# Kernel optimization log

Hardware: AMD Instinct MI355X
Metric: run time of the kernel (lower is better)

## Reference

```python
import jax, jax.numpy as jnp
import numpy as np

TAU = 0.07
EPS = 1e-6  # torch CosineSimilarity eps


def setup_inputs() -> dict:
    key = jax.random.key(0)
    k1, k2, k3 = jax.random.split(key, 3)
    n, d, n_classes = 8192, 256, 1024
    imitation_embeds = jax.random.normal(k1, (n, d), dtype=jnp.float32)
    recording_embeds = jax.random.normal(k2, (n, d), dtype=jnp.float32)
    labels = jax.random.randint(k3, (n,), 0, n_classes, dtype=jnp.int64)
    return {
        "imitation_embeds": imitation_embeds,
        "recording_embeds": recording_embeds,
        "labels": labels,
    }


def reference(imitation_embeds, recording_embeds, labels):
    n = imitation_embeds.shape[0]
    # cosine similarity with per-vector norm clamp (torch semantics)
    im_n = imitation_embeds / jnp.maximum(
        jnp.linalg.norm(imitation_embeds, axis=1, keepdims=True), EPS)
    rec_n = recording_embeds / jnp.maximum(
        jnp.linalg.norm(recording_embeds, axis=1, keepdims=True), EPS)
    i2r = jnp.einsum("nd,md->nm", im_n, rec_n) / TAU  # [n, n]

    same = labels[:, None] == labels[None, :]          # [n, n] bool
    eye = jnp.eye(n, dtype=bool)
    # original: mask = ~(same ^ diag_embed(diag(same))); diag(same) is all True
    # -> keep the diagonal (positive) and all different-label negatives
    mask = ~(same ^ eye)

    # per-row masked log-softmax evaluated at the diagonal entry:
    # log_softmax(row[mask])[pos_of_diag] = i2r[i,i] - logsumexp(row over mask)
    lse = jax.nn.logsumexp(jnp.where(mask, i2r, -jnp.inf), axis=1)  # [n]
    loss = -jnp.mean(jnp.diagonal(i2r) - lse)
    return loss
```

## Files before the change

kernel.cpp:

```cpp
#include <hip/hip_runtime.h>

#define N 8192
#define D 256
#define INV_TAU 14.285714285714286f
#define LOG2E 1.4426950408889634f
#define EPSN 1e-6f

#define RT 256
#define CT 32
#define CSPLIT 16
#define CPB (N / CSPLIT)
#define NTILES (CPB / CT)
#define MAXC 96

typedef unsigned int u32x4 __attribute__((ext_vector_type(4)));
typedef __bf16 bf16x8 __attribute__((ext_vector_type(8)));
typedef float f32x4 __attribute__((ext_vector_type(4)));

__device__ inline unsigned short f2bf(float x) {
    unsigned int u = __builtin_bit_cast(unsigned int, x);
    u += 0x7fffu + ((u >> 16) & 1u);
    return (unsigned short)(u >> 16);
}

__device__ inline float bf2f(unsigned short u) {
    return __builtin_bit_cast(float, (unsigned int)u << 16);
}

__global__ void ntx_prep(const float* __restrict__ im, const float* __restrict__ rec,
                         unsigned short* __restrict__ A, unsigned short* __restrict__ Bm,
                         float* __restrict__ diag, float* __restrict__ rowsum,
                         int* __restrict__ cnt, float* __restrict__ out) {
    const int wave = threadIdx.x >> 6;
    const int lane = threadIdx.x & 63;
    const int row  = blockIdx.x * 4 + wave;

    const float4 a = ((const float4*)(im  + (size_t)row * D))[lane];
    const float4 b = ((const float4*)(rec + (size_t)row * D))[lane];

    float ssa = a.x*a.x + a.y*a.y + a.z*a.z + a.w*a.w;
    float ssb = b.x*b.x + b.y*b.y + b.z*b.z + b.w*b.w;
    float dt  = a.x*b.x + a.y*b.y + a.z*b.z + a.w*b.w;
    #pragma unroll
    for (int o = 32; o; o >>= 1) {
        ssa += __shfl_xor(ssa, o);
        ssb += __shfl_xor(ssb, o);
        dt  += __shfl_xor(dt , o);
    }
    const float ra = 1.0f / fmaxf(sqrtf(ssa), EPSN);
    const float rb = 1.0f / fmaxf(sqrtf(ssb), EPSN);
    const float sa = ra * (INV_TAU * LOG2E);

    ushort4 pa, pb;
    pa.x = f2bf(a.x*sa); pa.y = f2bf(a.y*sa); pa.z = f2bf(a.z*sa); pa.w = f2bf(a.w*sa);
    pb.x = f2bf(b.x*rb); pb.y = f2bf(b.y*rb); pb.z = f2bf(b.z*rb); pb.w = f2bf(b.w*rb);
    *(ushort4*)(A  + (size_t)row * D + lane * 4) = pa;
    *(ushort4*)(Bm + (size_t)row * D + lane * 4) = pb;

    if (lane == 0) {
        diag[row]   = dt * ra * rb * INV_TAU;
        rowsum[row] = 0.0f;
    }
    if (blockIdx.x < 4) cnt[blockIdx.x * 256 + threadIdx.x] = 0;
    if (blockIdx.x == 0 && threadIdx.x == 0) out[0] = 0.0f;
}

__global__ void ntx_bucket(const int* __restrict__ labels, int* __restrict__ cnt,
                           int* __restrict__ bucket) {
    const int i = blockIdx.x * 256 + threadIdx.x;
    const int c = labels[i];
    const int pos = atomicAdd(&cnt[c], 1);
    if (pos < MAXC) bucket[c * MAXC + pos] = i;
}

__global__ void ntx_pairs(const unsigned short* __restrict__ A,
                          const unsigned short* __restrict__ Bm,
                          const int* __restrict__ labels,
                          const int* __restrict__ cnt, const int* __restrict__ bucket,
                          float* __restrict__ rowsum) {
    const int wave = threadIdx.x >> 6;
    const int lane = threadIdx.x & 63;
    const int i = blockIdx.x * 4 + wave;
    const int c = labels[i];
    const int m = min(cnt[c], MAXC);
    if (m < 2) return;

    const ushort4 av = *(const ushort4*)(A + (size_t)i * D + lane * 4);
    const float a0 = bf2f(av.x), a1 = bf2f(av.y), a2 = bf2f(av.z), a3 = bf2f(av.w);

    int jr_n = bucket[c * MAXC];
    ushort4 bv_n = *(const ushort4*)(Bm + (size_t)jr_n * D + lane * 4);

    float corr = 0.f;
    for (int j = 0; j < m; ++j) {
        const int jr = jr_n;
        const ushort4 bv = bv_n;
        if (j + 1 < m) {
            jr_n = bucket[c * MAXC + j + 1];
            bv_n = *(const ushort4*)(Bm + (size_t)jr_n * D + lane * 4);
        }
        if (jr == i) continue;
        float d = a0*bf2f(bv.x) + a1*bf2f(bv.y) + a2*bf2f(bv.z) + a3*bf2f(bv.w);
        #pragma unroll
        for (int o = 32; o; o >>= 1) d += __shfl_xor(d, o);
        corr += __builtin_amdgcn_exp2f(d);
    }
    if (lane == 0) atomicAdd(&rowsum[i], -corr);
}

__device__ __forceinline__ void stage_tile4(const unsigned short* __restrict__ Bm,
                                            int colt, int wave, int lane,
                                            unsigned char* lb) {
    const int g = lane >> 4, n16 = lane & 15;
    #pragma unroll
    for (int p = 0; p < 4; ++p) {
        const int csk = wave * 4 + p;
        const int cs = csk >> 3, k = csk & 7;
        const unsigned short* gs =
            Bm + (size_t)(colt + cs * 16 + n16) * D + k * 32 + g * 8;
        __builtin_amdgcn_global_load_lds(
            (const __attribute__((address_space(1))) unsigned int*)gs,
            (__attribute__((address_space(3))) unsigned int*)(lb + csk * 1024),
            16, 0, 0);
    }
}

template<bool STAGE>
__device__ __forceinline__ void tile_step(const unsigned short* __restrict__ Bm,
                                          int colstage, int wave, int lane,
                                          const unsigned char* cur, unsigned char* stg,
                                          const bf16x8 (&afrag)[4][8], float (&acc)[4][4]) {
    const int g = lane >> 4, n16 = lane & 15;
    #pragma unroll
    for (int cs = 0; cs < 2; ++cs) {
        if constexpr (STAGE) {
            #pragma unroll
            for (int p = cs * 2; p < cs * 2 + 2; ++p) {
                const int csk = wave * 4 + p;
                const int scs = csk >> 3, sk = csk & 7;
                const unsigned short* gs =
                    Bm + (size_t)(colstage + scs * 16 + n16) * D + sk * 32 + g * 8;
                __builtin_amdgcn_global_load_lds(
                    (const __attribute__((address_space(1))) unsigned int*)gs,
                    (__attribute__((address_space(3))) unsigned int*)(stg + csk * 1024),
                    16, 0, 0);
            }
        }
        bf16x8 bfrag[8];
        #pragma unroll
        for (int k = 0; k < 8; ++k)
            bfrag[k] = __builtin_bit_cast(
                bf16x8, *(const u32x4*)(cur + (cs * 8 + k) * 1024 + lane * 16));

        f32x4 c[4];
        __builtin_amdgcn_s_setprio(1);
        #pragma unroll
        for (int rs = 0; rs < 4; ++rs) {
            c[rs] = (f32x4){0.f, 0.f, 0.f, 0.f};
            #pragma unroll
            for (int k = 0; k < 8; ++k)
                c[rs] = __builtin_amdgcn_mfma_f32_16x16x32_bf16(
                            afrag[rs][k], bfrag[k], c[rs], 0, 0, 0);
        }
        __builtin_amdgcn_s_setprio(0);
        #pragma unroll
        for (int rs = 0; rs < 4; ++rs)
            #pragma unroll
            for (int q = 0; q < 4; ++q)
                acc[rs][q] += __builtin_amdgcn_exp2f(c[rs][q]);
    }
}

__global__ __launch_bounds__(256, 2)
void ntx_lse(const unsigned short* __restrict__ A, const unsigned short* __restrict__ Bm,
             float* __restrict__ rowsum) {
    __shared__ __align__(128) unsigned char Bs[3][CT * 512];

    const int wave = threadIdx.x >> 6;
    const int lane = threadIdx.x & 63;
    const int g    = lane >> 4;
    const int n16  = lane & 15;

    const int rowblk = blockIdx.x & (N / RT - 1);
    const int colblk = blockIdx.x >> 5;
    const int row0 = rowblk * RT + wave * 64;
    const int col0 = colblk * CPB;

    bf16x8 afrag[4][8];
    #pragma unroll
    for (int rs = 0; rs < 4; ++rs) {
        const int r = row0 + rs * 16 + n16;
        #pragma unroll
        for (int k = 0; k < 8; ++k)
            afrag[rs][k] = __builtin_bit_cast(
                bf16x8, *(const u32x4*)(A + (size_t)r * D + k * 32 + g * 8));
    }

    float acc[4][4];
    #pragma unroll
    for (int rs = 0; rs < 4; ++rs)
        #pragma unroll
        for (int q = 0; q < 4; ++q) acc[rs][q] = 0.f;

    unsigned char* b0 = &Bs[0][0];
    unsigned char* b1 = &Bs[1][0];
    unsigned char* b2 = &Bs[2][0];

    stage_tile4(Bm, col0,      wave, lane, b0);
    stage_tile4(Bm, col0 + CT, wave, lane, b1);

    for (int t = 0; t < NTILES - 1; ++t) {
        asm volatile("s_waitcnt vmcnt(4)" ::: "memory");
        __builtin_amdgcn_s_barrier();
        __builtin_amdgcn_sched_barrier(0);

        if (t + 2 < NTILES)
            tile_step<true >(Bm, col0 + (t + 2) * CT, wave, lane, b0, b2, afrag, acc);
        else
            tile_step<false>(Bm, 0, wave, lane, b0, b2, afrag, acc);

        unsigned char* tmp = b0; b0 = b1; b1 = b2; b2 = tmp;
    }
    asm volatile("s_waitcnt vmcnt(0)" ::: "memory");
    __builtin_amdgcn_s_barrier();
    __builtin_amdgcn_sched_barrier(0);
    tile_step<false>(Bm, 0, wave, lane, b0, b2, afrag, acc);

    #pragma unroll
    for (int rs = 0; rs < 4; ++rs)
        #pragma unroll
        for (int q = 0; q < 4; ++q) {
            float v = acc[rs][q];
            v += __shfl_xor(v, 1);
            v += __shfl_xor(v, 2);
            v += __shfl_xor(v, 4);
            v += __shfl_xor(v, 8);
            if (n16 == 0)
                atomicAdd(&rowsum[row0 + rs * 16 + g * 4 + q], v);
        }
}

__global__ void ntx_finish(const float* __restrict__ diag,
                           const float* __restrict__ rowsum,
                           float* __restrict__ out) {
    __shared__ float red[4];
    const int i = blockIdx.x * 256 + threadIdx.x;
    float s = logf(rowsum[i]) - diag[i];
    #pragma unroll
    for (int o = 32; o; o >>= 1) s += __shfl_xor(s, o);
    if ((threadIdx.x & 63) == 0) red[threadIdx.x >> 6] = s;
    __syncthreads();
    if (threadIdx.x == 0)
        atomicAdd(out, (red[0] + red[1] + red[2] + red[3]) * (1.0f / (float)N));
}

extern "C" void kernel_launch(void* const* d_in, const int* in_sizes, int n_in,
                              void* d_out, int out_size, void* d_ws, size_t ws_size,
                              hipStream_t stream) {
    const float* im     = (const float*)d_in[0];
    const float* rec    = (const float*)d_in[1];
    const int*   labels = (const int*)d_in[2];
    float* out = (float*)d_out;

    unsigned short* A  = (unsigned short*)d_ws;
    unsigned short* Bm = A + (size_t)N * D;
    float* diag   = (float*)(Bm + (size_t)N * D);
    float* rowsum = diag + N;
    int*   cnt    = (int*)(rowsum + N);
    int*   bucket = cnt + 1024;

    ntx_prep<<<N / 4, 256, 0, stream>>>(im, rec, A, Bm, diag, rowsum, cnt, out);
    ntx_bucket<<<N / 256, 256, 0, stream>>>(labels, cnt, bucket);
    ntx_pairs<<<N / 4, 256, 0, stream>>>(A, Bm, labels, cnt, bucket, rowsum);
    ntx_lse<<<(N / RT) * CSPLIT, 256, 0, stream>>>(A, Bm, rowsum);
    ntx_finish<<<N / 256, 256, 0, stream>>>(diag, rowsum, out);
}
```

Before: 121.0 us.

## Halve rows per wave and interleave MFMAs across column subtiles

```diff
diff --git a/kernel.cpp b/kernel.cpp
--- a/kernel.cpp
+++ b/kernel.cpp
@@ -6,9 +6,9 @@
 #define LOG2E 1.4426950408889634f
 #define EPSN 1e-6f
 
-#define RT 256
+#define RT 128
 #define CT 32
-#define CSPLIT 16
+#define CSPLIT 8
 #define CPB (N / CSPLIT)
 #define NTILES (CPB / CT)
 #define MAXC 96
@@ -129,46 +129,55 @@
 __device__ __forceinline__ void tile_step(const unsigned short* __restrict__ Bm,
                                           int colstage, int wave, int lane,
                                           const unsigned char* cur, unsigned char* stg,
-                                          const bf16x8 (&afrag)[4][8], float (&acc)[4][4]) {
+                                          const bf16x8 (&afrag)[2][8], float (&acc)[2][4]) {
     const int g = lane >> 4, n16 = lane & 15;
-    #pragma unroll
-    for (int cs = 0; cs < 2; ++cs) {
-        if constexpr (STAGE) {
+    if constexpr (STAGE) {
+        #pragma unroll
+        for (int p = 0; p < 4; ++p) {
+            const int csk = wave * 4 + p;
+            const int scs = csk >> 3, sk = csk & 7;
+            const unsigned short* gs =
+                Bm + (size_t)(colstage + scs * 16 + n16) * D + sk * 32 + g * 8;
+            __builtin_amdgcn_global_load_lds(
+                (const __attribute__((address_space(1))) unsigned int*)gs,
+                (__attribute__((address_space(3))) unsigned int*)(stg + csk * 1024),
+                16, 0, 0);
+        }
+    }
+
+    bf16x8 bfrag[2][8];
+    #pragma unroll
+    for (int cs = 0; cs < 2; ++cs)
+        #pragma unroll
+        for (int k = 0; k < 8; ++k)
+            bfrag[cs][k] = __builtin_bit_cast(
+                bf16x8, *(const u32x4*)(cur + (cs * 8 + k) * 1024 + lane * 16));
+
+    f32x4 c[2][2];
+    #pragma unroll
+    for (int cs = 0; cs < 2; ++cs)
+        #pragma unroll
+        for (int rs = 0; rs < 2; ++rs)
+            c[cs][rs] = (f32x4){0.f, 0.f, 0.f, 0.f};
+
+    __builtin_amdgcn_s_setprio(1);
+    #pragma unroll
+    for (int k = 0; k < 8; ++k)
+        #pragma unroll
+        for (int cs = 0; cs < 2; ++cs)
             #pragma unroll
-            for (int p = cs * 2; p < cs * 2 + 2; ++p) {
-                const int csk = wave * 4 + p;
-                const int scs = csk >> 3, sk = csk & 7;
-                const unsigned short* gs =
-                    Bm + (size_t)(colstage + scs * 16 + n16) * D + sk * 32 + g * 8;
-                __builtin_amdgcn_global_load_lds(
-                    (const __attribute__((address_space(1))) unsigned int*)gs,
-                    (__attribute__((address_space(3))) unsigned int*)(stg + csk * 1024),
-                    16, 0, 0);
-            }
-        }
-        bf16x8 bfrag[8];
-        #pragma unroll
-        for (int k = 0; k < 8; ++k)
-            bfrag[k] = __builtin_bit_cast(
-                bf16x8, *(const u32x4*)(cur + (cs * 8 + k) * 1024 + lane * 16));
-
-        f32x4 c[4];
-        __builtin_amdgcn_s_setprio(1);
-        #pragma unroll
-        for (int rs = 0; rs < 4; ++rs) {
-            c[rs] = (f32x4){0.f, 0.f, 0.f, 0.f};
-            #pragma unroll
-            for (int k = 0; k < 8; ++k)
-                c[rs] = __builtin_amdgcn_mfma_f32_16x16x32_bf16(
-                            afrag[rs][k], bfrag[k], c[rs], 0, 0, 0);
-        }
-        __builtin_amdgcn_s_setprio(0);
-        #pragma unroll
-        for (int rs = 0; rs < 4; ++rs)
+            for (int rs = 0; rs < 2; ++rs)
+                c[cs][rs] = __builtin_amdgcn_mfma_f32_16x16x32_bf16(
+                                afrag[rs][k], bfrag[cs][k], c[cs][rs], 0, 0, 0);
+    __builtin_amdgcn_s_setprio(0);
+
+    #pragma unroll
+    for (int cs = 0; cs < 2; ++cs)
+        #pragma unroll
+        for (int rs = 0; rs < 2; ++rs)
             #pragma unroll
             for (int q = 0; q < 4; ++q)
-                acc[rs][q] += __builtin_amdgcn_exp2f(c[rs][q]);
-    }
+                acc[rs][q] += __builtin_amdgcn_exp2f(c[cs][rs][q]);
 }
 
 __global__ __launch_bounds__(256, 2)
@@ -182,13 +191,13 @@
     const int n16  = lane & 15;
 
     const int rowblk = blockIdx.x & (N / RT - 1);
-    const int colblk = blockIdx.x >> 5;
-    const int row0 = rowblk * RT + wave * 64;
+    const int colblk = blockIdx.x >> 6;
+    const int row0 = rowblk * RT + wave * 32;
     const int col0 = colblk * CPB;
 
-    bf16x8 afrag[4][8];
-    #pragma unroll
-    for (int rs = 0; rs < 4; ++rs) {
+    bf16x8 afrag[2][8];
+    #pragma unroll
+    for (int rs = 0; rs < 2; ++rs) {
         const int r = row0 + rs * 16 + n16;
         #pragma unroll
         for (int k = 0; k < 8; ++k)
@@ -196,11 +205,7 @@
                 bf16x8, *(const u32x4*)(A + (size_t)r * D + k * 32 + g * 8));
     }
 
-    float acc[4][4];
-    #pragma unroll
-    for (int rs = 0; rs < 4; ++rs)
-        #pragma unroll
-        for (int q = 0; q < 4; ++q) acc[rs][q] = 0.f;
+    float acc[2][4] = {{0.f,0.f,0.f,0.f},{0.f,0.f,0.f,0.f}};
 
     unsigned char* b0 = &Bs[0][0];
     unsigned char* b1 = &Bs[1][0];
@@ -227,7 +232,7 @@
     tile_step<false>(Bm, 0, wave, lane, b0, b2, afrag, acc);
 
     #pragma unroll
-    for (int rs = 0; rs < 4; ++rs)
+    for (int rs = 0; rs < 2; ++rs)
         #pragma unroll
         for (int q = 0; q < 4; ++q) {
             float v = acc[rs][q];
```

New measurement: 123.0 us. About the same (+1.7%).
